# Optimization experiments

Hardware: AMD Instinct MI355X
Metric: run time of the kernel (lower is better)

## Reference

```python
import jax, jax.numpy as jnp
import numpy as np

B, N, W = 4, 4096, 1024
H, A, P = 16, 64, 64


def setup_inputs() -> dict:
    key = jax.random.key(0)
    ks = jax.random.split(key, 11)
    u = lambda k, shape: jax.random.uniform(k, shape, jnp.float32, -0.05, 0.05)  # keras 'random_uniform'
    glorot_v = (2.0 / (W + A)) ** 0.5
    return {
        'x': jax.random.normal(ks[0], (B, N, W), jnp.float32),
        'k1': u(ks[1], (H, W)),
        'k2': u(ks[2], (H, W)),
        'k3': u(ks[3], (H, W)),
        'a1': u(ks[4], (H, P, 1)),
        'a2': u(ks[5], (H, P, 1)),
        'b1': u(ks[6], (H, P, 1)),
        'b2': u(ks[7], (H, P, 1)),
        'c': u(ks[8], (H, P, 1)),
        'value_weight': jax.random.normal(ks[9], (H, W, A), jnp.float32) * glorot_v,
        'output_weight': jax.random.normal(ks[10], (H, W, A), jnp.float32) * glorot_v,
    }


def reference(x, k1, k2, k3, a1, a2, b1, b2, c, value_weight, output_weight):
    n = jnp.linspace(0.0, 1.0, x.shape[-2])                      # [N]
    p1 = jnp.sum(jnp.sin(a1 * n + b1) * c, axis=-2)              # [H,N]
    p2 = jnp.sum(jnp.sin(a2 * n + b2) * c, axis=-2)              # [H,N]
    cross = jnp.einsum('bnw,hw->bhn', x, k1) + p1                # [B,H,N]
    diag = jnp.einsum('bnw,hw->bhn', x, k2)
    extra = jnp.einsum('bnw,hw->bhn', x, k3)
    values = jnp.einsum('bnw,hwa->bhna', x, value_weight)        # [B,H,N,A]
    cexp = lambda z: jnp.exp(jnp.clip(z, -20.0, 20.0))[..., None]
    cross, diag, extra = cexp(cross), cexp(diag), cexp(extra)    # [B,H,N,1]
    p2e = cexp(p2)                                               # [H,N,1]
    num = jnp.cumsum(cross * values, axis=2) * p2e * extra + values * diag
    den = jnp.cumsum(cross, axis=2) * p2e * extra + diag
    out = num / den                                              # [B,H,N,A]
    return jnp.einsum('bhna,hwa->bnw', out, output_weight)       # [B,N,W]
```

## Files before the change

kernel.cpp:

```cpp
#include <hip/hip_runtime.h>
#include <hip/hip_bf16.h>
#include <stdint.h>

typedef __hip_bfloat16 bf16;
typedef __attribute__((ext_vector_type(8))) short short8;
typedef __attribute__((ext_vector_type(4))) float floatx4;

#define Bb 4
#define Nn 4096
#define Ww 1024
#define Hh 16
#define Aa 64
#define Pp 64
#define Jj 64
#define Ll 64

__device__ __forceinline__ float clamp20(float z){ return fminf(fmaxf(z, -20.0f), 20.0f); }
__device__ __forceinline__ float b2f(unsigned short u){ return __uint_as_float((unsigned)u << 16); }
__device__ __forceinline__ unsigned short f2b(float f){
    bf16 t = __float2bfloat16(f);
    return *reinterpret_cast<unsigned short*>(&t);
}

__device__ __forceinline__ void gl_lds16(const bf16* g, bf16* l){
    __builtin_amdgcn_global_load_lds((const __attribute__((address_space(1))) void*)g,
                                     (__attribute__((address_space(3))) void*)l, 16, 0, 0);
}


__global__ __launch_bounds__(256) void prep_w(
    const float* __restrict__ k1, const float* __restrict__ k2, const float* __restrict__ k3,
    const float* __restrict__ vw, const float* __restrict__ ow,
    bf16* __restrict__ Ktp, bf16* __restrict__ VWt, bf16* __restrict__ OWt){
    const int blk = blockIdx.x, tid = threadIdx.x;
    if (blk < 256){
        __shared__ float tile[64][65];
        const int h = blk >> 4, w0 = (blk & 15) * 64;
#pragma unroll
        for (int p = 0; p < 4; ++p){
            int wr = p * 16 + (tid >> 4);
            int a4 = (tid & 15) * 4;
            float4 v = *(const float4*)(vw + (h << 16) + ((w0 + wr) << 6) + a4);
            tile[wr][a4 + 0] = v.x; tile[wr][a4 + 1] = v.y;
            tile[wr][a4 + 2] = v.z; tile[wr][a4 + 3] = v.w;
        }
        __syncthreads();
#pragma unroll
        for (int p = 0; p < 4; ++p){
            int ar = p * 16 + (tid >> 4);
            int w4 = (tid & 15) * 4;
            ushort4 o = make_ushort4(f2b(tile[w4 + 0][ar]), f2b(tile[w4 + 1][ar]),
                                     f2b(tile[w4 + 2][ar]), f2b(tile[w4 + 3][ar]));
            *(ushort4*)(VWt + (size_t)(h * 64 + ar) * 1024 + w0 + w4) = o;
        }
    } else if (blk < 1280){
        int idx = (blk - 256) * 256 + tid;
        int base = idx * 4;
        int w = base >> 10, r0 = base & 1023;
        int h = r0 >> 6, a0 = r0 & 63;
        float4 v = *(const float4*)(ow + (h << 16) + (w << 6) + a0);
        *(ushort4*)(OWt + base) = make_ushort4(f2b(v.x), f2b(v.y), f2b(v.z), f2b(v.w));
    } else {
        int idx = (blk - 1280) * 256 + tid;
        int base = idx * 4;
        int r = base >> 10, k = base & 1023;
        float4 v = make_float4(0.f, 0.f, 0.f, 0.f);
        if (r < 16)      v = *(const float4*)(k1 + r * 1024 + k);
        else if (r < 32) v = *(const float4*)(k2 + (r - 16) * 1024 + k);
        else if (r < 48) v = *(const float4*)(k3 + (r - 32) * 1024 + k);
        *(ushort4*)(Ktp + base) = make_ushort4(f2b(v.x), f2b(v.y), f2b(v.z), f2b(v.w));
    }
}

__global__ __launch_bounds__(256) void prep_sin(
    const float* __restrict__ a1, const float* __restrict__ a2,
    const float* __restrict__ b1, const float* __restrict__ b2,
    const float* __restrict__ c,
    float* __restrict__ p1, float* __restrict__ p2e){
    __shared__ float sa1[64], sa2[64], sb1[64], sb2[64], scf[64];
    const int blk = blockIdx.x, tid = threadIdx.x;
    const int h = blk >> 4;
    if (tid < 64){
        sa1[tid] = a1[h * 64 + tid];
        sa2[tid] = a2[h * 64 + tid];
        sb1[tid] = b1[h * 64 + tid];
        sb2[tid] = b2[h * 64 + tid];
        scf[tid] = c [h * 64 + tid];
    }
    __syncthreads();
    const int idx = blk * 256 + tid;
    const int i = idx & (Nn - 1);
    float t = (float)i * (1.0f / (float)(Nn - 1));
    float s1 = 0.f, s2 = 0.f;
#pragma unroll 8
    for (int p = 0; p < Pp; ++p){
        float cv = scf[p];
        s1 += __sinf(sa1[p] * t + sb1[p]) * cv;
        s2 += __sinf(sa2[p] * t + sb2[p]) * cv;
    }
    p1[idx]  = s1;
    p2e[idx] = expf(clamp20(s2));
}

__global__ __launch_bounds__(256) void proj_gemm(const float* __restrict__ X,
                                                 const bf16* __restrict__ Ktp,
                                                 const float* __restrict__ p1,
                                                 bf16* __restrict__ xb,
                                                 float* __restrict__ cross_e,
                                                 float* __restrict__ diag_e,
                                                 float* __restrict__ extra_e){
    __shared__ bf16 Bs[2][48 * 128];
    const int tid  = threadIdx.x;
    const int wave = tid >> 6, lane = tid & 63;
    const int m0 = blockIdx.x * 64;
    const int fr = lane & 15, quad = lane >> 4;

    const float* Xf = X  + (size_t)(m0 + wave * 16 + fr) * 1024 + quad * 8;
    bf16*       xbf = xb + (size_t)(m0 + wave * 16 + fr) * 1024 + quad * 8;

    floatx4 acc[3] = {};
    float4 xA[8], xB[8];

    auto loadX = [&](float4 (&d)[8], int t){
#pragma unroll
        for (int i = 0; i < 4; ++i){
            d[2 * i]     = *(const float4*)(Xf + t * 128 + 32 * i);
            d[2 * i + 1] = *(const float4*)(Xf + t * 128 + 32 * i + 4);
        }
    };
    auto stageB = [&](int t){
        bf16* base = &Bs[t & 1][0];
#pragma unroll
        for (int s = 0; s < 3; ++s){
            int c = tid + s * 256;
            int row = c >> 4, pch = c & 15;
            int gcol = (pch ^ (row & 7)) << 3;
            gl_lds16(Ktp + (size_t)row * 1024 + t * 128 + gcol,
                     base + (size_t)(wave * 64 + s * 256) * 8);
        }
    };
    auto iter = [&](int t, float4 (&xc_)[8], int vmN){
        if (vmN == 0)       asm volatile("s_waitcnt vmcnt(0)"  ::: "memory");
        else if (vmN == 11) asm volatile("s_waitcnt vmcnt(11)" ::: "memory");
        else                asm volatile("s_waitcnt vmcnt(15)" ::: "memory");
        __builtin_amdgcn_sched_barrier(0);
        short8 afr[4];
#pragma unroll
        for (int i = 0; i < 4; ++i){
            union { ushort4 u4[2]; short8 s8; } pk;
            pk.u4[0] = make_ushort4(f2b(xc_[2*i].x),   f2b(xc_[2*i].y),
                                    f2b(xc_[2*i].z),   f2b(xc_[2*i].w));
            pk.u4[1] = make_ushort4(f2b(xc_[2*i+1].x), f2b(xc_[2*i+1].y),
                                    f2b(xc_[2*i+1].z), f2b(xc_[2*i+1].w));
            afr[i] = pk.s8;
            *(short8*)(xbf + t * 128 + i * 32) = pk.s8;
        }
        __builtin_amdgcn_sched_barrier(0);
        __builtin_amdgcn_s_barrier();
        __builtin_amdgcn_sched_barrier(0);
        short8 bfr[3][4];
#pragma unroll
        for (int j = 0; j < 3; ++j)
#pragma unroll
            for (int i = 0; i < 4; ++i){
                int R = j * 16 + fr;
                int pch = (4 * i + quad) ^ (R & 7);
                bfr[j][i] = *(const short8*)&Bs[t & 1][R * 128 + pch * 8];
            }
        asm volatile("s_waitcnt lgkmcnt(0)" ::: "memory");
        __builtin_amdgcn_sched_barrier(0);
        __builtin_amdgcn_s_barrier();
        __builtin_amdgcn_sched_barrier(0);
        if (t + 2 < 8){ loadX(xc_, t + 2); stageB(t + 2); }
        __builtin_amdgcn_sched_barrier(0);
#pragma unroll
        for (int i = 0; i < 4; ++i)
#pragma unroll
            for (int j = 0; j < 3; ++j)
                acc[j] = __builtin_amdgcn_mfma_f32_16x16x32_bf16(afr[i], bfr[j][i], acc[j], 0, 0, 0);
    };

    loadX(xA, 0); stageB(0);
    loadX(xB, 1); stageB(1);
    __builtin_amdgcn_sched_barrier(0);

#pragma unroll
    for (int tt = 0; tt < 4; ++tt){
        iter(2 * tt,     xA, (tt == 0) ? 11 : 15);
        iter(2 * tt + 1, xB, (tt == 3) ? 0  : 15);
    }

    const int cr = quad * 4;
#pragma unroll
    for (int j = 0; j < 3; ++j){
        float* dst = (j == 0) ? cross_e : (j == 1) ? diag_e : extra_e;
#pragma unroll
        for (int r = 0; r < 4; ++r){
            int row = m0 + wave * 16 + cr + r;
            int n = row & (Nn - 1), b = row >> 12;
            float s = acc[j][r];
            if (j == 0) s += p1[fr * Nn + n];
            dst[(b * Hh + fr) * Nn + n] = expf(clamp20(s));
        }
    }
}

__device__ __forceinline__ void stage_q(const bf16* srcTileBase, int K, bf16* ldsQuarter, int tid){
    int r  = tid >> 3;
    int col = (((tid & 7) ^ (r & 7)) << 3);
    gl_lds16(srcTileBase + (size_t)r * K + col, ldsQuarter + (tid >> 6) * 512);
}

template<int WRITE_BF16>
__global__ __launch_bounds__(512) void gemm256(const bf16* __restrict__ A,
                                               const bf16* __restrict__ Bt,
                                               void* __restrict__ Cv,
                                               int M, int N, int K){
    __shared__ bf16 ldsA[2][256 * 64];
    __shared__ bf16 ldsB[2][256 * 64];
    const int tid  = threadIdx.x;
    const int wave = tid >> 6, lane = tid & 63;

    const int flat = blockIdx.y * gridDim.x + blockIdx.x;
    const int nwg  = gridDim.x * gridDim.y;
    const int cpx  = nwg >> 3;
    const int swz  = (flat & 7) * cpx + (flat >> 3);
    const int m0 = (swz / gridDim.x) * 256, n0 = (swz % gridDim.x) * 256;
    const int wm = (wave >> 2) * 128, wn = (wave & 3) * 64;
    const int fr = lane & 15, quad = lane >> 4;
    const int nt = K >> 6;

    floatx4 acc[8][4] = {};

#pragma unroll
    for (int q = 0; q < 4; ++q)
        stage_q(A  + (size_t)(m0 + q * 64) * K, K, &ldsA[0][q * 4096], tid);
#pragma unroll
    for (int q = 0; q < 4; ++q)
        stage_q(Bt + (size_t)(n0 + q * 64) * K, K, &ldsB[0][q * 4096], tid);
#pragma unroll
    for (int q = 0; q < 4; ++q)
        stage_q(Bt + (size_t)(n0 + q * 64) * K + 64, K, &ldsB[1][q * 4096], tid);
    stage_q(A + (size_t)(m0 +   0) * K + 64, K, &ldsA[1][0 * 4096], tid);
    stage_q(A + (size_t)(m0 + 128) * K + 64, K, &ldsA[1][2 * 4096], tid);

    for (int t = 0; t < nt; ++t){
        if (t == nt - 1) asm volatile("s_waitcnt vmcnt(0)" ::: "memory");
        else             asm volatile("s_waitcnt vmcnt(6)" ::: "memory");
        __builtin_amdgcn_sched_barrier(0);
        __builtin_amdgcn_s_barrier();
        __builtin_amdgcn_sched_barrier(0);

        const bf16* Abuf = ldsA[t & 1];
        const bf16* Bbuf = ldsB[t & 1];
        short8 bfr[4][2];

#pragma unroll
        for (int p = 0; p < 4; ++p){
            short8 af[2][2];
#pragma unroll
            for (int ii = 0; ii < 2; ++ii){
                int R = wm + (2 * p + ii) * 16 + fr;
#pragma unroll
                for (int kc = 0; kc < 2; ++kc){
                    int lb = kc * 4 + quad;
                    af[ii][kc] = *(const short8*)&Abuf[R * 64 + ((lb ^ (R & 7)) << 3)];
                }
            }
            if (p == 0){
#pragma unroll
                for (int j = 0; j < 4; ++j){
                    int R = wn + j * 16 + fr;
#pragma unroll
                    for (int kc = 0; kc < 2; ++kc){
                        int lb = kc * 4 + quad;
                        bfr[j][kc] = *(const short8*)&Bbuf[R * 64 + ((lb ^ (R & 7)) << 3)];
                    }
                }
            }
            if (p == 0 && t + 1 < nt){
                bf16* d = ldsA[(t + 1) & 1];
                stage_q(A + (size_t)(m0 +  64) * K + (size_t)(t + 1) * 64, K, d + 1 * 4096, tid);
                stage_q(A + (size_t)(m0 + 192) * K + (size_t)(t + 1) * 64, K, d + 3 * 4096, tid);
            }
            if (p == 1 && t + 2 < nt){
                bf16* d = ldsB[t & 1];
                stage_q(Bt + (size_t)(n0 +   0) * K + (size_t)(t + 2) * 64, K, d + 0 * 4096, tid);
                stage_q(Bt + (size_t)(n0 +  64) * K + (size_t)(t + 2) * 64, K, d + 1 * 4096, tid);
            }
            if (p == 2 && t + 2 < nt){
                bf16* d = ldsB[t & 1];
                stage_q(Bt + (size_t)(n0 + 128) * K + (size_t)(t + 2) * 64, K, d + 2 * 4096, tid);
                stage_q(Bt + (size_t)(n0 + 192) * K + (size_t)(t + 2) * 64, K, d + 3 * 4096, tid);
            }
            if (p == 3 && t + 2 < nt){
                bf16* d = ldsA[t & 1];
                stage_q(A + (size_t)(m0 +   0) * K + (size_t)(t + 2) * 64, K, d + 0 * 4096, tid);
                stage_q(A + (size_t)(m0 + 128) * K + (size_t)(t + 2) * 64, K, d + 2 * 4096, tid);
            }
            __builtin_amdgcn_s_setprio(1);
#pragma unroll
            for (int ii = 0; ii < 2; ++ii)
#pragma unroll
                for (int j = 0; j < 4; ++j)
#pragma unroll
                    for (int kc = 0; kc < 2; ++kc)
                        acc[2 * p + ii][j] = __builtin_amdgcn_mfma_f32_16x16x32_bf16(
                            af[ii][kc], bfr[j][kc], acc[2 * p + ii][j], 0, 0, 0);
            __builtin_amdgcn_s_setprio(0);
            if (p == 0 || p == 1){
                __builtin_amdgcn_s_barrier();
                __builtin_amdgcn_sched_barrier(0);
            }
        }
    }

    const int cr = quad * 4;
#pragma unroll
    for (int i = 0; i < 8; ++i)
#pragma unroll
        for (int j = 0; j < 4; ++j){
            int row = m0 + wm + i * 16 + cr;
            int col = n0 + wn + j * 16 + fr;
            if (WRITE_BF16){
                bf16* C = (bf16*)Cv;
#pragma unroll
                for (int r = 0; r < 4; ++r)
                    C[(size_t)(row + r) * N + col] = __float2bfloat16(acc[i][j][r]);
            } else {
                float* C = (float*)Cv;
#pragma unroll
                for (int r = 0; r < 4; ++r)
                    C[(size_t)(row + r) * N + col] = acc[i][j][r];
            }
        }
}

__global__ __launch_bounds__(64) void scan1(const bf16* __restrict__ values,
                                            const float* __restrict__ cross_e,
                                            float* __restrict__ csum_c, float* __restrict__ csum_cv){
    const int blk = blockIdx.x;
    const int j = blk & (Jj - 1);
    const int bh = blk >> 6;
    const int h = bh & (Hh - 1), b = bh >> 4;
    const int lane = threadIdx.x;
    const int tq = lane >> 4;
    const int a4 = (lane & 15) << 2;
    const float* cp = cross_e + bh * Nn + j * Ll;
    float sc = 0.f, s0 = 0.f, s1 = 0.f, s2 = 0.f, s3 = 0.f;
#pragma unroll
    for (int i = 0; i < 16; ++i){
        int t = tq * 16 + i;
        int n = j * Ll + t;
        float ce = cp[t];
        ushort4 pv = *(const ushort4*)(values + (((size_t)(b * Nn + n)) << 10) + (h << 6) + a4);
        sc += ce;
        s0 += ce * b2f(pv.x); s1 += ce * b2f(pv.y);
        s2 += ce * b2f(pv.z); s3 += ce * b2f(pv.w);
    }
    sc += __shfl_xor(sc, 16); sc += __shfl_xor(sc, 32);
    s0 += __shfl_xor(s0, 16); s0 += __shfl_xor(s0, 32);
    s1 += __shfl_xor(s1, 16); s1 += __shfl_xor(s1, 32);
    s2 += __shfl_xor(s2, 16); s2 += __shfl_xor(s2, 32);
    s3 += __shfl_xor(s3, 16); s3 += __shfl_xor(s3, 32);
    if (lane == 0) csum_c[blk] = sc;
    if (tq == 0){
        float4 o = make_float4(s0, s1, s2, s3);
        *(float4*)(csum_cv + (blk << 6) + a4) = o;
    }
}

__global__ __launch_bounds__(64) void scan2(const float* __restrict__ csum_c,
                                            const float* __restrict__ csum_cv,
                                            float* __restrict__ pref_c, float* __restrict__ pref_cv){
    const int bh = blockIdx.x;
    const int lane = threadIdx.x;
    float rc = 0.f, rcv = 0.f;
    for (int j = 0; j < Jj; ++j){
        int idx = bh * Jj + j;
        if (lane == 0) pref_c[idx] = rc;
        pref_cv[(idx << 6) + lane] = rcv;
        rc  += csum_c[idx];
        rcv += csum_cv[(idx << 6) + lane];
    }
}

__global__ __launch_bounds__(64) void scan3(const bf16* __restrict__ values,
                                            const float* __restrict__ cross_e,
                                            const float* __restrict__ diag_e,
                                            const float* __restrict__ extra_e,
                                            const float* __restrict__ p2e,
                                            const float* __restrict__ pref_c,
                                            const float* __restrict__ pref_cv,
                                            bf16* __restrict__ out2){
    const int blk = blockIdx.x;
    const int j = blk & (Jj - 1);
    const int bh = blk >> 6;
    const int h = bh & (Hh - 1), b = bh >> 4;
    const int lane = threadIdx.x;
    const int tq = lane >> 4;
    const int al = lane & 15;
    const int a4 = al << 2;
    const float* cp = cross_e + bh * Nn + j * Ll;
    const float* dp = diag_e  + bh * Nn + j * Ll;
    const float* ep = extra_e + bh * Nn + j * Ll;
    const float* pp = p2e + h * Nn + j * Ll;

    ushort4 pv[16];
    float cef[16];
    float lc = 0.f, l0 = 0.f, l1 = 0.f, l2 = 0.f, l3 = 0.f;
#pragma unroll
    for (int i = 0; i < 16; ++i){
        int t = tq * 16 + i;
        int n = j * Ll + t;
        cef[i] = cp[t];
        pv[i] = *(const ushort4*)(values + (((size_t)(b * Nn + n)) << 10) + (h << 6) + a4);
        float ce = cef[i];
        lc += ce;
        l0 += ce * b2f(pv[i].x); l1 += ce * b2f(pv[i].y);
        l2 += ce * b2f(pv[i].z); l3 += ce * b2f(pv[i].w);
    }

    float rc = pref_c[blk];
    float4 pcv = *(const float4*)(pref_cv + (blk << 6) + a4);
    float r0 = pcv.x, r1 = pcv.y, r2 = pcv.z, r3 = pcv.w;
#pragma unroll
    for (int g = 0; g < 3; ++g){
        int src = g * 16 + al;
        float oc = __shfl(lc, src);
        float o0 = __shfl(l0, src), o1 = __shfl(l1, src);
        float o2 = __shfl(l2, src), o3 = __shfl(l3, src);
        if (tq > g){ rc += oc; r0 += o0; r1 += o1; r2 += o2; r3 += o3; }
    }

#pragma unroll
    for (int i = 0; i < 16; ++i){
        int t = tq * 16 + i;
        int n = j * Ll + t;
        float ce = cef[i], de = dp[t], ee = ep[t], pe = pp[t];
        float v0 = b2f(pv[i].x), v1 = b2f(pv[i].y);
        float v2 = b2f(pv[i].z), v3 = b2f(pv[i].w);
        rc += ce;
        r0 += ce * v0; r1 += ce * v1; r2 += ce * v2; r3 += ce * v3;
        float pee = pe * ee;
        float invd = 1.0f / (rc * pee + de);
        ushort4 o;
        o.x = f2b((r0 * pee + v0 * de) * invd);
        o.y = f2b((r1 * pee + v1 * de) * invd);
        o.z = f2b((r2 * pee + v2 * de) * invd);
        o.w = f2b((r3 * pee + v3 * de) * invd);
        *(ushort4*)(out2 + (((size_t)(b * Nn + n)) << 10) + (h << 6) + a4) = o;
    }
}

extern "C" void kernel_launch(void* const* d_in, const int* in_sizes, int n_in,
                              void* d_out, int out_size, void* d_ws, size_t ws_size,
                              hipStream_t stream){
    const float* x  = (const float*)d_in[0];
    const float* k1 = (const float*)d_in[1];
    const float* k2 = (const float*)d_in[2];
    const float* k3 = (const float*)d_in[3];
    const float* a1 = (const float*)d_in[4];
    const float* a2 = (const float*)d_in[5];
    const float* b1 = (const float*)d_in[6];
    const float* b2 = (const float*)d_in[7];
    const float* c  = (const float*)d_in[8];
    const float* vw = (const float*)d_in[9];
    const float* ow = (const float*)d_in[10];
    float* out = (float*)d_out;

    char* p = (char*)d_ws;
    auto alloc = [&](size_t bytes) -> void* {
        void* r = (void*)p;
        p += (bytes + 255) & ~(size_t)255;
        return r;
    };
    bf16*  xb      = (bf16*) alloc((size_t)Bb * Nn * Ww * 2);
    bf16*  Ktp     = (bf16*) alloc((size_t)64 * Ww * 2);
    bf16*  VWt     = (bf16*) alloc((size_t)Hh * Aa * Ww * 2);
    bf16*  OWt     = (bf16*) alloc((size_t)Ww * Hh * Aa * 2);
    float* p1      = (float*)alloc((size_t)Hh * Nn * 4);
    float* p2e     = (float*)alloc((size_t)Hh * Nn * 4);
    float* cross_e = (float*)alloc((size_t)Bb * Hh * Nn * 4);
    float* diag_e  = (float*)alloc((size_t)Bb * Hh * Nn * 4);
    float* extra_e = (float*)alloc((size_t)Bb * Hh * Nn * 4);
    float* csum_c  = (float*)alloc((size_t)Bb * Hh * Jj * 4);
    float* pref_c  = (float*)alloc((size_t)Bb * Hh * Jj * 4);
    float* csum_cv = (float*)alloc((size_t)Bb * Hh * Jj * Aa * 4);
    float* pref_cv = (float*)alloc((size_t)Bb * Hh * Jj * Aa * 4);
    bf16*  values  = (bf16*) alloc((size_t)Bb * Nn * Hh * Aa * 2);
    bf16*  out2    = (bf16*) alloc((size_t)Bb * Nn * Hh * Aa * 2);

    prep_w  <<<1344, 256, 0, stream>>>(k1, k2, k3, vw, ow, Ktp, VWt, OWt);
    prep_sin<<<256, 256, 0, stream>>>(a1, a2, b1, b2, c, p1, p2e);
    proj_gemm<<<(Bb * Nn) / 64, 256, 0, stream>>>(x, Ktp, p1, xb, cross_e, diag_e, extra_e);
    gemm256<1><<<dim3((Hh * Aa) / 256, (Bb * Nn) / 256), 512, 0, stream>>>(xb, VWt, (void*)values, Bb * Nn, Hh * Aa, Ww);
    scan1<<<Bb * Hh * Jj, 64, 0, stream>>>(values, cross_e, csum_c, csum_cv);
    scan2<<<Bb * Hh, 64, 0, stream>>>(csum_c, csum_cv, pref_c, pref_cv);
    scan3<<<Bb * Hh * Jj, 64, 0, stream>>>(values, cross_e, diag_e, extra_e, p2e, pref_c, pref_cv, out2);
    gemm256<0><<<dim3(Ww / 256, (Bb * Nn) / 256), 512, 0, stream>>>(out2, OWt, (void*)out, Bb * Nn, Ww, Hh * Aa);
}
```

Measured before the change: 257.7 us.

## Fuse chunk-sum scan pass into value GEMM epilogue

```diff
diff --git a/kernel.cpp b/kernel.cpp
--- a/kernel.cpp
+++ b/kernel.cpp
@@ -215,6 +215,9 @@
 __global__ __launch_bounds__(512) void gemm256(const bf16* __restrict__ A,
                                                const bf16* __restrict__ Bt,
                                                void* __restrict__ Cv,
+                                               const float* __restrict__ cross_e,
+                                               float* __restrict__ csum_c,
+                                               float* __restrict__ csum_cv,
                                                int M, int N, int K){
     __shared__ bf16 ldsA[2][256 * 64];
     __shared__ bf16 ldsB[2][256 * 64];
@@ -334,39 +337,53 @@
                     C[(size_t)(row + r) * N + col] = acc[i][j][r];
             }
         }
-}
-
-__global__ __launch_bounds__(64) void scan1(const bf16* __restrict__ values,
-                                            const float* __restrict__ cross_e,
-                                            float* __restrict__ csum_c, float* __restrict__ csum_cv){
-    const int blk = blockIdx.x;
-    const int j = blk & (Jj - 1);
-    const int bh = blk >> 6;
-    const int h = bh & (Hh - 1), b = bh >> 4;
-    const int lane = threadIdx.x;
-    const int tq = lane >> 4;
-    const int a4 = (lane & 15) << 2;
-    const float* cp = cross_e + bh * Nn + j * Ll;
-    float sc = 0.f, s0 = 0.f, s1 = 0.f, s2 = 0.f, s3 = 0.f;
-#pragma unroll
-    for (int i = 0; i < 16; ++i){
-        int t = tq * 16 + i;
-        int n = j * Ll + t;
-        float ce = cp[t];
-        ushort4 pv = *(const ushort4*)(values + (((size_t)(b * Nn + n)) << 10) + (h << 6) + a4);
-        sc += ce;
-        s0 += ce * b2f(pv.x); s1 += ce * b2f(pv.y);
-        s2 += ce * b2f(pv.z); s3 += ce * b2f(pv.w);
-    }
-    sc += __shfl_xor(sc, 16); sc += __shfl_xor(sc, 32);
-    s0 += __shfl_xor(s0, 16); s0 += __shfl_xor(s0, 32);
-    s1 += __shfl_xor(s1, 16); s1 += __shfl_xor(s1, 32);
-    s2 += __shfl_xor(s2, 16); s2 += __shfl_xor(s2, 32);
-    s3 += __shfl_xor(s3, 16); s3 += __shfl_xor(s3, 32);
-    if (lane == 0) csum_c[blk] = sc;
-    if (tq == 0){
-        float4 o = make_float4(s0, s1, s2, s3);
-        *(float4*)(csum_cv + (blk << 6) + a4) = o;
+
+    if (WRITE_BF16){
+        __syncthreads();
+        float* crossLds = (float*)&ldsA[0][0];
+        const int b  = m0 >> 12;
+        const int nb = m0 & (Nn - 1);
+#pragma unroll
+        for (int s = 0; s < 2; ++s){
+            int idx = tid + s * 512;
+            int hh = idx >> 8, nn = idx & 255;
+            crossLds[hh * 256 + nn] =
+                cross_e[(size_t)((b << 4) + (n0 >> 6) + hh) * Nn + nb + nn];
+        }
+        __syncthreads();
+        const int hl = wn >> 6;
+        const int bh = (b << 4) + (n0 >> 6) + hl;
+#pragma unroll
+        for (int cc = 0; cc < 2; ++cc){
+            float sj[4] = {0.f, 0.f, 0.f, 0.f};
+#pragma unroll
+            for (int i = 0; i < 4; ++i){
+                int ii = cc * 4 + i;
+#pragma unroll
+                for (int r = 0; r < 4; ++r){
+                    float cw = crossLds[hl * 256 + wm + ii * 16 + quad * 4 + r];
+#pragma unroll
+                    for (int j = 0; j < 4; ++j)
+                        sj[j] += cw * acc[ii][j][r];
+                }
+            }
+#pragma unroll
+            for (int j = 0; j < 4; ++j){
+                sj[j] += __shfl_xor(sj[j], 16);
+                sj[j] += __shfl_xor(sj[j], 32);
+            }
+            const int jg = (nb >> 6) + (wm >> 6) + cc;
+            if (quad == 0){
+#pragma unroll
+                for (int j = 0; j < 4; ++j)
+                    csum_cv[((size_t)(bh * Jj + jg) << 6) + j * 16 + fr] = sj[j];
+            }
+            float vc = crossLds[hl * 256 + wm + cc * 64 + lane];
+            vc += __shfl_xor(vc, 1);  vc += __shfl_xor(vc, 2);
+            vc += __shfl_xor(vc, 4);  vc += __shfl_xor(vc, 8);
+            vc += __shfl_xor(vc, 16); vc += __shfl_xor(vc, 32);
+            if (lane == 0) csum_c[bh * Jj + jg] = vc;
+        }
     }
 }
 
@@ -494,9 +511,10 @@
     prep_w  <<<1344, 256, 0, stream>>>(k1, k2, k3, vw, ow, Ktp, VWt, OWt);
     prep_sin<<<256, 256, 0, stream>>>(a1, a2, b1, b2, c, p1, p2e);
     proj_gemm<<<(Bb * Nn) / 64, 256, 0, stream>>>(x, Ktp, p1, xb, cross_e, diag_e, extra_e);
-    gemm256<1><<<dim3((Hh * Aa) / 256, (Bb * Nn) / 256), 512, 0, stream>>>(xb, VWt, (void*)values, Bb * Nn, Hh * Aa, Ww);
-    scan1<<<Bb * Hh * Jj, 64, 0, stream>>>(values, cross_e, csum_c, csum_cv);
+    gemm256<1><<<dim3((Hh * Aa) / 256, (Bb * Nn) / 256), 512, 0, stream>>>(
+        xb, VWt, (void*)values, cross_e, csum_c, csum_cv, Bb * Nn, Hh * Aa, Ww);
     scan2<<<Bb * Hh, 64, 0, stream>>>(csum_c, csum_cv, pref_c, pref_cv);
     scan3<<<Bb * Hh * Jj, 64, 0, stream>>>(values, cross_e, diag_e, extra_e, p2e, pref_c, pref_cv, out2);
-    gemm256<0><<<dim3(Ww / 256, (Bb * Nn) / 256), 512, 0, stream>>>(out2, OWt, (void*)out, Bb * Nn, Ww, Hh * Aa);
-}
+    gemm256<0><<<dim3(Ww / 256, (Bb * Nn) / 256), 512, 0, stream>>>(
+        out2, OWt, (void*)out, nullptr, nullptr, nullptr, Bb * Nn, Ww, Hh * Aa);
+}
```

New measurement: 255.7 us. About the same (-0.8%).
